# Kernel tuning notes

Measured on AMD Instinct MI355X. Metric: run time of the kernel, lower is better.

The kernel has to match this reference:

```python
import jax, jax.numpy as jnp
import numpy as np

T = 1024      # tokens
H = 2048      # hidden_size
I = 1408      # moe_intermediate_size
E = 16        # n_routed_experts
K = 6         # num_experts_per_tok
SI = I * 2    # shared experts intermediate (n_shared_experts=2)


def setup_inputs() -> dict:
    key = jax.random.key(0)
    ks = jax.random.split(key, 8)
    s = 0.02
    return {
        "x": jax.random.normal(ks[0], (T, H), jnp.float32),
        "gate_w": jax.random.normal(ks[1], (E, H), jnp.float32) * s,
        "w_gate": jax.random.normal(ks[2], (E, I, H), jnp.float32) * s,
        "w_up": jax.random.normal(ks[3], (E, I, H), jnp.float32) * s,
        "w_down": jax.random.normal(ks[4], (E, H, I), jnp.float32) * s,
        "sw_gate": jax.random.normal(ks[5], (SI, H), jnp.float32) * s,
        "sw_up": jax.random.normal(ks[6], (SI, H), jnp.float32) * s,
        "sw_down": jax.random.normal(ks[7], (H, SI), jnp.float32) * s,
    }


def reference(x, gate_w, w_gate, w_up, w_down, sw_gate, sw_up, sw_down):
    t = x.shape[0]
    # ---- router: softmax over experts, top-k, renormalize (norm_topk_prob) ----
    logits = x @ gate_w.T                                   # [T, E]
    probs = jax.nn.softmax(logits.astype(jnp.float32), axis=-1)
    topw, topi = jax.lax.top_k(probs, K)                    # [T, K]
    topw = topw / jnp.sum(topw, axis=-1, keepdims=True)
    # per-token per-expert combine weight (0 for unselected experts)
    comb = jnp.zeros((t, E), probs.dtype).at[
        jnp.arange(t)[:, None], topi
    ].add(topw)                                             # [T, E]

    # ---- routed experts: SwiGLU MLP per expert, weighted combine ----
    g = jnp.einsum('th,eih->tei', x, w_gate)                # [T, E, I]
    u = jnp.einsum('th,eih->tei', x, w_up)                  # [T, E, I]
    h = jax.nn.silu(g) * u                                  # [T, E, I]
    routed = jnp.einsum('te,tei,ehi->th', comb, h, w_down)  # [T, H]

    # ---- shared experts (always-on SwiGLU MLP) ----
    shared = (jax.nn.silu(x @ sw_gate.T) * (x @ sw_up.T)) @ sw_down.T  # [T, H]

    return routed + shared
```

## Files before the change

### kernel.cpp

```cpp
#include <hip/hip_runtime.h>
#include <stdint.h>

#define T_TOK 1024
#define H_DIM 2048
#define I_DIM 1408
#define E_NUM 16
#define K_TOP 6
#define SI_DIM 2816
#define PADCAP 8192

typedef __attribute__((ext_vector_type(8))) short short8;
typedef __attribute__((ext_vector_type(8))) unsigned short ushort8;
typedef __attribute__((ext_vector_type(4))) float f32x4;

__device__ __forceinline__ unsigned short f2b(float f) {
    unsigned u = __float_as_uint(f);
    u += 0x7fffu + ((u >> 16) & 1u);
    return (unsigned short)(u >> 16);
}
__device__ __forceinline__ float b2f(unsigned short s) {
    return __uint_as_float((unsigned)s << 16);
}

__device__ __forceinline__ unsigned cvt_pk2(float a, float b) {
    unsigned r;
    asm("v_cvt_pk_bf16_f32 %0, %1, %2" : "=v"(r) : "v"(a), "v"(b));
    return r;
}

typedef __attribute__((address_space(1))) const unsigned int as1_uint;
typedef __attribute__((address_space(3))) unsigned int as3_uint;
__device__ __forceinline__ void gload16(const void* g, void* l) {
    __builtin_amdgcn_global_load_lds((as1_uint*)g, (as3_uint*)l, 16, 0, 0);
}

__device__ __forceinline__ int xcd_swizzle(int bid, int nwg) {
    const int q = nwg >> 3, r = nwg & 7;
    const int xcd = bid & 7, k = bid >> 3;
    const int base = (xcd < r) ? xcd * (q + 1) : r * (q + 1) + (xcd - r) * q;
    return base + k;
}

__global__ __launch_bounds__(256) void router_kernel(
    const float* __restrict__ x, const float* __restrict__ gw,
    float* __restrict__ topw, int* __restrict__ eidx, int* __restrict__ slotarr,
    int* __restrict__ counts)
{
    const int t = blockIdx.x, tid = threadIdx.x;
    const int lane = tid & 63, wave = tid >> 6;
    float part[E_NUM];
#pragma unroll
    for (int e = 0; e < E_NUM; ++e) part[e] = 0.f;
    const float* xr = x + (size_t)t * H_DIM;
    for (int i = tid; i < H_DIM; i += 256) {
        float xv = xr[i];
#pragma unroll
        for (int e = 0; e < E_NUM; ++e) part[e] += xv * gw[e * H_DIM + i];
    }
    __shared__ float red[4][E_NUM];
#pragma unroll
    for (int e = 0; e < E_NUM; ++e) {
        float v = part[e];
        for (int off = 32; off; off >>= 1) v += __shfl_down(v, off);
        if (lane == 0) red[wave][e] = v;
    }
    __syncthreads();
    if (tid == 0) {
        float logits[E_NUM];
#pragma unroll
        for (int e = 0; e < E_NUM; ++e)
            logits[e] = red[0][e] + red[1][e] + red[2][e] + red[3][e];
        int sel[K_TOP]; float selv[K_TOP];
        unsigned used = 0;
        for (int k = 0; k < K_TOP; ++k) {
            int best = 0; float bv = -1e30f;
            for (int e = 0; e < E_NUM; ++e)
                if (!((used >> e) & 1u) && logits[e] > bv) { bv = logits[e]; best = e; }
            used |= 1u << best; sel[k] = best; selv[k] = bv;
        }
        float mx = selv[0], s = 0.f, w[K_TOP];
        for (int k = 0; k < K_TOP; ++k) { w[k] = expf(selv[k] - mx); s += w[k]; }
        float inv = 1.f / s;
        for (int k = 0; k < K_TOP; ++k) {
            int slot = atomicAdd(&counts[sel[k]], 1);
            topw[t * K_TOP + k] = w[k] * inv;
            eidx[t * K_TOP + k] = sel[k];
            slotarr[t * K_TOP + k] = slot;
        }
    }
}

__global__ void zero_counts_kernel(int* counts) {
    if (threadIdx.x < E_NUM) counts[threadIdx.x] = 0;
}

__global__ void prefix_kernel(const int* __restrict__ counts, int* __restrict__ offs) {
    if (threadIdx.x == 0) {
        int o = 0;
        for (int e = 0; e < E_NUM; ++e) { offs[e] = o; o += (counts[e] + 127) & ~127; }
        offs[E_NUM] = o;
    }
}

__global__ __launch_bounds__(256) void gather_rows_kernel(
    const float* __restrict__ x, const int* __restrict__ eidx,
    const int* __restrict__ slotarr, const int* __restrict__ offs,
    ushort* __restrict__ Xg)
{
    const int b = blockIdx.x;
    const int t = b / K_TOP;
    const int e = eidx[b], s = slotarr[b];
    const size_t row = (size_t)offs[e] + (size_t)s;
    const float* src = x + (size_t)t * H_DIM;
    ushort* dst = Xg + row * H_DIM;
    const int i = threadIdx.x * 8;
    float4 f0 = *(const float4*)(src + i);
    float4 f1 = *(const float4*)(src + i + 4);
    ushort8 v;
    v[0] = f2b(f0.x); v[1] = f2b(f0.y); v[2] = f2b(f0.z); v[3] = f2b(f0.w);
    v[4] = f2b(f1.x); v[5] = f2b(f1.y); v[6] = f2b(f1.z); v[7] = f2b(f1.w);
    *(ushort8*)(dst + i) = v;
}

__global__ __launch_bounds__(256) void cvt_rows_kernel(
    const float* __restrict__ x, ushort* __restrict__ Xb)
{
    const size_t row = blockIdx.x;
    const float* src = x + row * H_DIM;
    ushort* dst = Xb + row * H_DIM;
    const int i = threadIdx.x * 8;
    float4 f0 = *(const float4*)(src + i);
    float4 f1 = *(const float4*)(src + i + 4);
    ushort8 v;
    v[0] = f2b(f0.x); v[1] = f2b(f0.y); v[2] = f2b(f0.z); v[3] = f2b(f0.w);
    v[4] = f2b(f1.x); v[5] = f2b(f1.y); v[6] = f2b(f1.z); v[7] = f2b(f1.w);
    *(ushort8*)(dst + i) = v;
}

template<int STORE_F32>
__global__ __launch_bounds__(256) void gemm_bt_kernel(
    const ushort* __restrict__ Abase,
    const float* __restrict__ B1, const float* __restrict__ B2,
    void* __restrict__ C1, void* __restrict__ C2,
    const int* __restrict__ counts, const int* __restrict__ offs,
    int Mconst, int nNT, int totNT, int nMT, int K, long strideB, int ldc)
{
    __shared__ short Alds[128 * 64];
    __shared__ float Blds[128 * 64];

    const int work = xcd_swizzle(blockIdx.x, gridDim.x);
    const int perE = totNT * nMT;
    const int e = work / perE;
    int rem = work - e * perE;
    int nt = rem / nMT;
    const int mt = rem - nt * nMT;

    int M = Mconst, rowbase = 0;
    if (counts) { M = counts[e]; rowbase = offs[e]; }
    const int row0 = mt * 128;
    if (row0 >= M) return;

    const float* Bsel = B1;
    void* Csel = C1;
    if (nt >= nNT) { Bsel = B2; Csel = C2; nt -= nNT; }
    const int n0 = nt * 128;
    const float* __restrict__ B = Bsel + (size_t)e * (size_t)strideB;
    const char* __restrict__ Ab = (const char*)(Abase + (size_t)(rowbase + row0) * K);
    const char* __restrict__ Bb = (const char*)(B + (size_t)n0 * K);

    const int tid = threadIdx.x;
    const int lane = tid & 63;
    const int wave = tid >> 6;
    const int wm = wave & 1, wn = wave >> 1;
    const int l15 = lane & 15, lhi = lane >> 4;

    int aRow[4], aSlot[4];
    char* aDst[4];
#pragma unroll
    for (int i = 0; i < 4; ++i) {
        const int chunk = wave * 4 + i;
        const int off = chunk * 1024 + lane * 16;
        const int r = off >> 7, s = (off >> 4) & 7;
        aRow[i] = r; aSlot[i] = s ^ (r & 7);
        aDst[i] = (char*)Alds + chunk * 1024;
    }
    int bRow[8], bSlot[8];
    char* bDst[8];
#pragma unroll
    for (int i = 0; i < 8; ++i) {
        const int chunk = wave * 8 + i;
        const int off = chunk * 1024 + lane * 16;
        const int r = off >> 8, s = (off >> 4) & 15;
        bRow[i] = r; bSlot[i] = s ^ (r & 7);
        bDst[i] = (char*)Blds + chunk * 1024;
    }

    f32x4 acc[4][4];
#pragma unroll
    for (int m = 0; m < 4; ++m)
#pragma unroll
        for (int n = 0; n < 4; ++n) acc[m][n] = (f32x4){0.f, 0.f, 0.f, 0.f};

    const int nK = K >> 6;
    for (int kt = 0; kt < nK; ++kt) {
        const int k0 = kt << 6;
        __syncthreads();
#pragma unroll
        for (int i = 0; i < 4; ++i)
            gload16(Ab + (size_t)aRow[i] * K * 2 + k0 * 2 + (aSlot[i] << 4), aDst[i]);
#pragma unroll
        for (int i = 0; i < 8; ++i)
            gload16(Bb + (size_t)bRow[i] * K * 4 + k0 * 4 + (bSlot[i] << 4), bDst[i]);
        __syncthreads();

#pragma unroll
        for (int kk = 0; kk < 2; ++kk) {
            const int kb = (kk << 2) + lhi;
            short8 af[4], bfr[4];
#pragma unroll
            for (int m = 0; m < 4; ++m) {
                const int rA = (wm << 6) + (m << 4) + l15;
                af[m] = *(const short8*)&Alds[(rA << 6) + ((kb ^ (rA & 7)) << 3)];
            }
#pragma unroll
            for (int n = 0; n < 4; ++n) {
                const int rB = (wn << 6) + (n << 4) + l15;
                const int s0 = (kb << 1) ^ (rB & 7);
                const int s1 = ((kb << 1) | 1) ^ (rB & 7);
                f32x4 x0 = *(const f32x4*)&Blds[(rB << 6) + (s0 << 2)];
                f32x4 x1 = *(const f32x4*)&Blds[(rB << 6) + (s1 << 2)];
                union { short8 s8; unsigned u[4]; } bb;
                bb.u[0] = cvt_pk2(x0[0], x0[1]);
                bb.u[1] = cvt_pk2(x0[2], x0[3]);
                bb.u[2] = cvt_pk2(x1[0], x1[1]);
                bb.u[3] = cvt_pk2(x1[2], x1[3]);
                bfr[n] = bb.s8;
            }
#pragma unroll
            for (int m = 0; m < 4; ++m)
#pragma unroll
                for (int n = 0; n < 4; ++n)
                    acc[m][n] = __builtin_amdgcn_mfma_f32_16x16x32_bf16(
                        af[m], bfr[n], acc[m][n], 0, 0, 0);
        }
    }

    const size_t cbase_col = (size_t)n0 + (wn << 6) + l15;
#pragma unroll
    for (int m = 0; m < 4; ++m) {
        const int rloc = (wm << 6) + (m << 4) + (lhi << 2);
#pragma unroll
        for (int j = 0; j < 4; ++j) {
            const int crow = row0 + rloc + j;
            if (crow >= M) continue;
            const size_t co = (size_t)(rowbase + crow) * ldc + cbase_col;
            if (STORE_F32) {
                float* C = (float*)Csel;
#pragma unroll
                for (int n = 0; n < 4; ++n) C[co + (n << 4)] = acc[m][n][j];
            } else {
                ushort* C = (ushort*)Csel;
#pragma unroll
                for (int n = 0; n < 4; ++n) C[co + (n << 4)] = f2b(acc[m][n][j]);
            }
        }
    }
}

__global__ __launch_bounds__(256) void silu_rows_kernel(
    const ushort* __restrict__ G, const ushort* __restrict__ U,
    ushort* __restrict__ Hh, const int* __restrict__ eidx,
    const int* __restrict__ slotarr, const int* __restrict__ offs, int rowlen)
{
    size_t row;
    if (eidx) {
        const int b = blockIdx.x;
        row = (size_t)offs[eidx[b]] + (size_t)slotarr[b];
    } else {
        row = blockIdx.x;
    }
    const ushort* g = G + row * rowlen;
    const ushort* u = U + row * rowlen;
    ushort* h = Hh + row * rowlen;
    for (int i = threadIdx.x * 8; i < rowlen; i += 2048) {
        ushort8 gv = *(const ushort8*)(g + i);
        ushort8 uv = *(const ushort8*)(u + i);
        ushort8 hv;
#pragma unroll
        for (int j = 0; j < 8; ++j) {
            float gf = b2f(gv[j]);
            float uf = b2f(uv[j]);
            float sf = gf / (1.f + expf(-gf));
            hv[j] = f2b(sf * uf);
        }
        *(ushort8*)(h + i) = hv;
    }
}

__global__ __launch_bounds__(256) void combine_kernel(
    float* __restrict__ out, const ushort* __restrict__ Y,
    const float* __restrict__ topw, const int* __restrict__ eidx,
    const int* __restrict__ slotarr, const int* __restrict__ offs)
{
    const int t = blockIdx.x;
    const int i = threadIdx.x * 8;
    float* o = out + (size_t)t * H_DIM;
    float acc[8];
    float4 o0 = *(const float4*)(o + i);
    float4 o1 = *(const float4*)(o + i + 4);
    acc[0] = o0.x; acc[1] = o0.y; acc[2] = o0.z; acc[3] = o0.w;
    acc[4] = o1.x; acc[5] = o1.y; acc[6] = o1.z; acc[7] = o1.w;
#pragma unroll
    for (int k = 0; k < K_TOP; ++k) {
        const float w = topw[t * K_TOP + k];
        const size_t row = (size_t)offs[eidx[t * K_TOP + k]] + (size_t)slotarr[t * K_TOP + k];
        ushort8 v = *(const ushort8*)(Y + row * H_DIM + i);
#pragma unroll
        for (int j = 0; j < 8; ++j) acc[j] += w * b2f(v[j]);
    }
    o0.x = acc[0]; o0.y = acc[1]; o0.z = acc[2]; o0.w = acc[3];
    o1.x = acc[4]; o1.y = acc[5]; o1.z = acc[6]; o1.w = acc[7];
    *(float4*)(o + i) = o0;
    *(float4*)(o + i + 4) = o1;
}

extern "C" void kernel_launch(void* const* d_in, const int* in_sizes, int n_in,
                              void* d_out, int out_size, void* d_ws, size_t ws_size,
                              hipStream_t stream) {
    const float* x       = (const float*)d_in[0];
    const float* gate_w  = (const float*)d_in[1];
    const float* w_gate  = (const float*)d_in[2];
    const float* w_up    = (const float*)d_in[3];
    const float* w_down  = (const float*)d_in[4];
    const float* sw_gate = (const float*)d_in[5];
    const float* sw_up   = (const float*)d_in[6];
    const float* sw_down = (const float*)d_in[7];
    float* out = (float*)d_out;

    char* p = (char*)d_ws;
    auto take = [&](size_t b) { char* r = p; p += (b + 255) & ~(size_t)255; return r; };
    int*    counts = (int*)take(E_NUM * 4);
    int*    offs   = (int*)take((E_NUM + 1) * 4);
    float*  topw   = (float*)take((size_t)T_TOK * K_TOP * 4);
    int*    eidx   = (int*)take((size_t)T_TOK * K_TOP * 4);
    int*    slot   = (int*)take((size_t)T_TOK * K_TOP * 4);
    ushort* Xg     = (ushort*)take((size_t)PADCAP * H_DIM * 2);
    ushort* G      = (ushort*)take((size_t)PADCAP * I_DIM * 2);
    ushort* U      = (ushort*)take((size_t)PADCAP * I_DIM * 2);
    ushort* Hr     = (ushort*)take((size_t)PADCAP * I_DIM * 2);
    ushort* Xb     = (ushort*)take((size_t)T_TOK * H_DIM * 2);
    ushort* Gs     = (ushort*)take((size_t)T_TOK * SI_DIM * 2);
    ushort* Us     = (ushort*)take((size_t)T_TOK * SI_DIM * 2);
    ushort* Hs     = (ushort*)take((size_t)T_TOK * SI_DIM * 2);

    zero_counts_kernel<<<1, 64, 0, stream>>>(counts);
    router_kernel<<<T_TOK, 256, 0, stream>>>(x, gate_w, topw, eidx, slot, counts);
    prefix_kernel<<<1, 64, 0, stream>>>(counts, offs);
    gather_rows_kernel<<<T_TOK * K_TOP, 256, 0, stream>>>(x, eidx, slot, offs, Xg);
    cvt_rows_kernel<<<T_TOK, 256, 0, stream>>>(x, Xb);

    gemm_bt_kernel<0><<<E_NUM * 22 * 8, 256, 0, stream>>>(
        Xg, w_gate, w_up, G, U, counts, offs,
        0, 11, 22, 8, H_DIM, (long)I_DIM * H_DIM, I_DIM);
    silu_rows_kernel<<<T_TOK * K_TOP, 256, 0, stream>>>(G, U, Hr, eidx, slot, offs, I_DIM);
    gemm_bt_kernel<0><<<E_NUM * 16 * 8, 256, 0, stream>>>(
        Hr, w_down, nullptr, Xg, nullptr, counts, offs,
        0, 16, 16, 8, I_DIM, (long)H_DIM * I_DIM, H_DIM);

    gemm_bt_kernel<0><<<44 * 8, 256, 0, stream>>>(
        Xb, sw_gate, sw_up, Gs, Us, nullptr, nullptr,
        T_TOK, 22, 44, 8, H_DIM, 0, SI_DIM);
    silu_rows_kernel<<<T_TOK, 256, 0, stream>>>(Gs, Us, Hs, nullptr, nullptr, nullptr, SI_DIM);
    gemm_bt_kernel<1><<<16 * 8, 256, 0, stream>>>(
        Hs, sw_down, nullptr, out, nullptr, nullptr, nullptr,
        T_TOK, 16, 16, 8, SI_DIM, 0, H_DIM);

    combine_kernel<<<T_TOK, 256, 0, stream>>>(out, Xg, topw, eidx, slot, offs);
}
```

Baseline: 553.8 us.

## Fold shared experts into grouped MoE GEMMs as two extra experts with register-staged B

Treats the two shared-expert halves as extra experts 16 and 17, so gate/up, SiLU and down projections run in single grouped launches instead of separate routed and shared kernels. The shared down projection writes two bf16 partial outputs that the combine kernel sums with the routed results. The GEMM now loads fp32 weights into registers and converts them to bf16 once per tile, writing a double-buffered bf16 LDS tile, rather than converting at every fragment read. This also prefetches the next K-tile during the MFMAs, cuts LDS traffic and sets occupancy to 3 blocks. SiLU writes in place and the gather and convert kernels are merged, at the cost of a bf16 round trip on the shared output and more workspace.

```diff
diff --git a/kernel.cpp b/kernel.cpp
--- a/kernel.cpp
+++ b/kernel.cpp
@@ -6,8 +6,8 @@
 #define I_DIM 1408
 #define E_NUM 16
 #define K_TOP 6
-#define SI_DIM 2816
 #define PADCAP 8192
+#define NE_ALL 18
 
 typedef __attribute__((ext_vector_type(8))) short short8;
 typedef __attribute__((ext_vector_type(8))) unsigned short ushort8;
@@ -102,17 +102,22 @@
     }
 }
 
-__global__ __launch_bounds__(256) void gather_rows_kernel(
+__global__ __launch_bounds__(256) void gather_cvt_kernel(
     const float* __restrict__ x, const int* __restrict__ eidx,
     const int* __restrict__ slotarr, const int* __restrict__ offs,
-    ushort* __restrict__ Xg)
+    ushort* __restrict__ Xall)
 {
     const int b = blockIdx.x;
-    const int t = b / K_TOP;
-    const int e = eidx[b], s = slotarr[b];
-    const size_t row = (size_t)offs[e] + (size_t)s;
+    int t; size_t row;
+    if (b < T_TOK * K_TOP) {
+        t = b / K_TOP;
+        row = (size_t)offs[eidx[b]] + (size_t)slotarr[b];
+    } else {
+        t = b - T_TOK * K_TOP;
+        row = (size_t)offs[E_NUM] + (size_t)t;
+    }
     const float* src = x + (size_t)t * H_DIM;
-    ushort* dst = Xg + row * H_DIM;
+    ushort* dst = Xall + row * H_DIM;
     const int i = threadIdx.x * 8;
     float4 f0 = *(const float4*)(src + i);
     float4 f1 = *(const float4*)(src + i + 4);
@@ -122,51 +127,48 @@
     *(ushort8*)(dst + i) = v;
 }
 
-__global__ __launch_bounds__(256) void cvt_rows_kernel(
-    const float* __restrict__ x, ushort* __restrict__ Xb)
-{
-    const size_t row = blockIdx.x;
-    const float* src = x + row * H_DIM;
-    ushort* dst = Xb + row * H_DIM;
-    const int i = threadIdx.x * 8;
-    float4 f0 = *(const float4*)(src + i);
-    float4 f1 = *(const float4*)(src + i + 4);
-    ushort8 v;
-    v[0] = f2b(f0.x); v[1] = f2b(f0.y); v[2] = f2b(f0.z); v[3] = f2b(f0.w);
-    v[4] = f2b(f1.x); v[5] = f2b(f1.y); v[6] = f2b(f1.z); v[7] = f2b(f1.w);
-    *(ushort8*)(dst + i) = v;
-}
-
-template<int STORE_F32>
-__global__ __launch_bounds__(256) void gemm_bt_kernel(
+template<int DOWN>
+__global__ __launch_bounds__(256, 3) void moe_gemm_kernel(
     const ushort* __restrict__ Abase,
-    const float* __restrict__ B1, const float* __restrict__ B2,
-    void* __restrict__ C1, void* __restrict__ C2,
+    const float* __restrict__ Wr1, const float* __restrict__ Wr2,
+    const float* __restrict__ Ws1, const float* __restrict__ Ws2,
+    ushort* __restrict__ C1, ushort* __restrict__ C2,
     const int* __restrict__ counts, const int* __restrict__ offs,
-    int Mconst, int nNT, int totNT, int nMT, int K, long strideB, int ldc)
+    int nNT, int K, int ldc)
 {
     __shared__ short Alds[128 * 64];
-    __shared__ float Blds[128 * 64];
+    __shared__ short Blds[2][128 * 64];
 
     const int work = xcd_swizzle(blockIdx.x, gridDim.x);
-    const int perE = totNT * nMT;
-    const int e = work / perE;
-    int rem = work - e * perE;
-    int nt = rem / nMT;
-    const int mt = rem - nt * nMT;
-
-    int M = Mconst, rowbase = 0;
-    if (counts) { M = counts[e]; rowbase = offs[e]; }
-    const int row0 = mt * 128;
+    const int slab = NE_ALL * 8;
+    int nt = work / slab;
+    const int rem = work - nt * slab;
+    const int e = rem >> 3;
+    const int mt = rem & 7;
+
+    const int S = offs[E_NUM];
+    const int M = (e < E_NUM) ? counts[e] : 1024;
+    const int row0 = mt << 7;
     if (row0 >= M) return;
-
-    const float* Bsel = B1;
-    void* Csel = C1;
-    if (nt >= nNT) { Bsel = B2; Csel = C2; nt -= nNT; }
-    const int n0 = nt * 128;
-    const float* __restrict__ B = Bsel + (size_t)e * (size_t)strideB;
-    const char* __restrict__ Ab = (const char*)(Abase + (size_t)(rowbase + row0) * K);
-    const char* __restrict__ Bb = (const char*)(B + (size_t)n0 * K);
+    const int crowbase = (e < E_NUM) ? offs[e] : S + ((e - E_NUM) << 10);
+    const int arowbase = DOWN ? crowbase : ((e < E_NUM) ? offs[e] : S);
+
+    const float* B; ushort* C; int ldb;
+    if (DOWN) {
+        ldb = (e < E_NUM) ? I_DIM : 2 * I_DIM;
+        B = (e < E_NUM) ? Wr1 + (size_t)e * H_DIM * I_DIM
+                        : Ws1 + (size_t)(e - E_NUM) * I_DIM;
+        C = C1;
+    } else {
+        ldb = H_DIM;
+        const float* Bg = (e < E_NUM) ? Wr1 + (size_t)e * I_DIM * H_DIM
+                                      : Ws1 + (size_t)(e - E_NUM) * I_DIM * H_DIM;
+        const float* Bu = (e < E_NUM) ? Wr2 + (size_t)e * I_DIM * H_DIM
+                                      : Ws2 + (size_t)(e - E_NUM) * I_DIM * H_DIM;
+        if (nt < nNT) { B = Bg; C = C1; }
+        else          { B = Bu; C = C2; nt -= nNT; }
+    }
+    const int n0 = nt << 7;
 
     const int tid = threadIdx.x;
     const int lane = tid & 63;
@@ -174,26 +176,22 @@
     const int wm = wave & 1, wn = wave >> 1;
     const int l15 = lane & 15, lhi = lane >> 4;
 
-    int aRow[4], aSlot[4];
-    char* aDst[4];
+    const char* __restrict__ Ab = (const char*)(Abase + (size_t)(arowbase + row0) * K);
+
+    int aOff[4]; char* aDst[4];
 #pragma unroll
     for (int i = 0; i < 4; ++i) {
         const int chunk = wave * 4 + i;
         const int off = chunk * 1024 + lane * 16;
         const int r = off >> 7, s = (off >> 4) & 7;
-        aRow[i] = r; aSlot[i] = s ^ (r & 7);
+        aOff[i] = r * K * 2 + ((s ^ (r & 7)) << 4);
         aDst[i] = (char*)Alds + chunk * 1024;
     }
-    int bRow[8], bSlot[8];
-    char* bDst[8];
-#pragma unroll
-    for (int i = 0; i < 8; ++i) {
-        const int chunk = wave * 8 + i;
-        const int off = chunk * 1024 + lane * 16;
-        const int r = off >> 8, s = (off >> 4) & 15;
-        bRow[i] = r; bSlot[i] = s ^ (r & 7);
-        bDst[i] = (char*)Blds + chunk * 1024;
-    }
+
+    const int r0 = (wave << 5) + (lane >> 3);
+    const int sl = lane & 7;
+    const float* Bg0 = B + (size_t)(n0 + r0) * ldb + (sl << 3);
+    const int bLds0 = (r0 << 6) + ((sl ^ (r0 & 7)) << 3);
 
     f32x4 acc[4][4];
 #pragma unroll
@@ -201,18 +199,40 @@
 #pragma unroll
         for (int n = 0; n < 4; ++n) acc[m][n] = (f32x4){0.f, 0.f, 0.f, 0.f};
 
+    float4 breg[4][2];
+    auto issueB = [&](int k0) {
+#pragma unroll
+        for (int j = 0; j < 4; ++j) {
+            const float* src = Bg0 + (size_t)(j << 3) * ldb + k0;
+            breg[j][0] = *(const float4*)src;
+            breg[j][1] = *(const float4*)(src + 4);
+        }
+    };
+    auto writeB = [&](int p) {
+        short* bl = Blds[p];
+#pragma unroll
+        for (int j = 0; j < 4; ++j) {
+            union { short8 s; unsigned u[4]; } w;
+            w.u[0] = cvt_pk2(breg[j][0].x, breg[j][0].y);
+            w.u[1] = cvt_pk2(breg[j][0].z, breg[j][0].w);
+            w.u[2] = cvt_pk2(breg[j][1].x, breg[j][1].y);
+            w.u[3] = cvt_pk2(breg[j][1].z, breg[j][1].w);
+            *(short8*)&bl[bLds0 + (j << 9)] = w.s;
+        }
+    };
+
     const int nK = K >> 6;
+    issueB(0);
+    int p = 0;
     for (int kt = 0; kt < nK; ++kt) {
         const int k0 = kt << 6;
         __syncthreads();
 #pragma unroll
         for (int i = 0; i < 4; ++i)
-            gload16(Ab + (size_t)aRow[i] * K * 2 + k0 * 2 + (aSlot[i] << 4), aDst[i]);
-#pragma unroll
-        for (int i = 0; i < 8; ++i)
-            gload16(Bb + (size_t)bRow[i] * K * 4 + k0 * 4 + (bSlot[i] << 4), bDst[i]);
+            gload16(Ab + (size_t)aOff[i] + k0 * 2, aDst[i]);
+        writeB(p);
         __syncthreads();
-
+        if (kt + 1 < nK) issueB(k0 + 64);
 #pragma unroll
         for (int kk = 0; kk < 2; ++kk) {
             const int kb = (kk << 2) + lhi;
@@ -225,16 +245,7 @@
 #pragma unroll
             for (int n = 0; n < 4; ++n) {
                 const int rB = (wn << 6) + (n << 4) + l15;
-                const int s0 = (kb << 1) ^ (rB & 7);
-                const int s1 = ((kb << 1) | 1) ^ (rB & 7);
-                f32x4 x0 = *(const f32x4*)&Blds[(rB << 6) + (s0 << 2)];
-                f32x4 x1 = *(const f32x4*)&Blds[(rB << 6) + (s1 << 2)];
-                union { short8 s8; unsigned u[4]; } bb;
-                bb.u[0] = cvt_pk2(x0[0], x0[1]);
-                bb.u[1] = cvt_pk2(x0[2], x0[3]);
-                bb.u[2] = cvt_pk2(x1[0], x1[1]);
-                bb.u[3] = cvt_pk2(x1[2], x1[3]);
-                bfr[n] = bb.s8;
+                bfr[n] = *(const short8*)&Blds[p][(rB << 6) + ((kb ^ (rB & 7)) << 3)];
             }
 #pragma unroll
             for (int m = 0; m < 4; ++m)
@@ -243,6 +254,7 @@
                     acc[m][n] = __builtin_amdgcn_mfma_f32_16x16x32_bf16(
                         af[m], bfr[n], acc[m][n], 0, 0, 0);
         }
+        p ^= 1;
     }
 
     const size_t cbase_col = (size_t)n0 + (wn << 6) + l15;
@@ -253,36 +265,28 @@
         for (int j = 0; j < 4; ++j) {
             const int crow = row0 + rloc + j;
             if (crow >= M) continue;
-            const size_t co = (size_t)(rowbase + crow) * ldc + cbase_col;
-            if (STORE_F32) {
-                float* C = (float*)Csel;
-#pragma unroll
-                for (int n = 0; n < 4; ++n) C[co + (n << 4)] = acc[m][n][j];
-            } else {
-                ushort* C = (ushort*)Csel;
-#pragma unroll
-                for (int n = 0; n < 4; ++n) C[co + (n << 4)] = f2b(acc[m][n][j]);
-            }
-        }
-    }
-}
-
-__global__ __launch_bounds__(256) void silu_rows_kernel(
-    const ushort* __restrict__ G, const ushort* __restrict__ U,
-    ushort* __restrict__ Hh, const int* __restrict__ eidx,
-    const int* __restrict__ slotarr, const int* __restrict__ offs, int rowlen)
-{
+            const size_t co = (size_t)(crowbase + crow) * ldc + cbase_col;
+#pragma unroll
+            for (int n = 0; n < 4; ++n) C[co + (n << 4)] = f2b(acc[m][n][j]);
+        }
+    }
+}
+
+__global__ __launch_bounds__(256) void silu_kernel(
+    ushort* __restrict__ G, const ushort* __restrict__ U,
+    const int* __restrict__ eidx, const int* __restrict__ slotarr,
+    const int* __restrict__ offs)
+{
+    const int b = blockIdx.x;
     size_t row;
-    if (eidx) {
-        const int b = blockIdx.x;
+    if (b < T_TOK * K_TOP) {
         row = (size_t)offs[eidx[b]] + (size_t)slotarr[b];
     } else {
-        row = blockIdx.x;
-    }
-    const ushort* g = G + row * rowlen;
-    const ushort* u = U + row * rowlen;
-    ushort* h = Hh + row * rowlen;
-    for (int i = threadIdx.x * 8; i < rowlen; i += 2048) {
+        row = (size_t)offs[E_NUM] + (size_t)(b - T_TOK * K_TOP);
+    }
+    ushort* g = G + row * I_DIM;
+    const ushort* u = U + row * I_DIM;
+    for (int i = threadIdx.x * 8; i < I_DIM; i += 2048) {
         ushort8 gv = *(const ushort8*)(g + i);
         ushort8 uv = *(const ushort8*)(u + i);
         ushort8 hv;
@@ -293,7 +297,7 @@
             float sf = gf / (1.f + expf(-gf));
             hv[j] = f2b(sf * uf);
         }
-        *(ushort8*)(h + i) = hv;
+        *(ushort8*)(g + i) = hv;
     }
 }
 
@@ -304,12 +308,14 @@
 {
     const int t = blockIdx.x;
     const int i = threadIdx.x * 8;
-    float* o = out + (size_t)t * H_DIM;
+    const int S = offs[E_NUM];
     float acc[8];
-    float4 o0 = *(const float4*)(o + i);
-    float4 o1 = *(const float4*)(o + i + 4);
-    acc[0] = o0.x; acc[1] = o0.y; acc[2] = o0.z; acc[3] = o0.w;
-    acc[4] = o1.x; acc[5] = o1.y; acc[6] = o1.z; acc[7] = o1.w;
+    {
+        ushort8 v0 = *(const ushort8*)(Y + ((size_t)S + t) * H_DIM + i);
+        ushort8 v1 = *(const ushort8*)(Y + ((size_t)S + 1024 + t) * H_DIM + i);
+#pragma unroll
+        for (int j = 0; j < 8; ++j) acc[j] = b2f(v0[j]) + b2f(v1[j]);
+    }
 #pragma unroll
     for (int k = 0; k < K_TOP; ++k) {
         const float w = topw[t * K_TOP + k];
@@ -318,6 +324,8 @@
 #pragma unroll
         for (int j = 0; j < 8; ++j) acc[j] += w * b2f(v[j]);
     }
+    float* o = out + (size_t)t * H_DIM;
+    float4 o0, o1;
     o0.x = acc[0]; o0.y = acc[1]; o0.z = acc[2]; o0.w = acc[3];
     o1.x = acc[4]; o1.y = acc[5]; o1.z = acc[6]; o1.w = acc[7];
     *(float4*)(o + i) = o0;
@@ -339,41 +347,26 @@
 
     char* p = (char*)d_ws;
     auto take = [&](size_t b) { char* r = p; p += (b + 255) & ~(size_t)255; return r; };
-    int*    counts = (int*)take(E_NUM * 4);
-    int*    offs   = (int*)take((E_NUM + 1) * 4);
+    int*    counts = (int*)take(32 * 4);
+    int*    offs   = (int*)take(32 * 4);
     float*  topw   = (float*)take((size_t)T_TOK * K_TOP * 4);
     int*    eidx   = (int*)take((size_t)T_TOK * K_TOP * 4);
     int*    slot   = (int*)take((size_t)T_TOK * K_TOP * 4);
-    ushort* Xg     = (ushort*)take((size_t)PADCAP * H_DIM * 2);
-    ushort* G      = (ushort*)take((size_t)PADCAP * I_DIM * 2);
-    ushort* U      = (ushort*)take((size_t)PADCAP * I_DIM * 2);
-    ushort* Hr     = (ushort*)take((size_t)PADCAP * I_DIM * 2);
-    ushort* Xb     = (ushort*)take((size_t)T_TOK * H_DIM * 2);
-    ushort* Gs     = (ushort*)take((size_t)T_TOK * SI_DIM * 2);
-    ushort* Us     = (ushort*)take((size_t)T_TOK * SI_DIM * 2);
-    ushort* Hs     = (ushort*)take((size_t)T_TOK * SI_DIM * 2);
+    ushort* Xall   = (ushort*)take((size_t)(PADCAP + 1024) * H_DIM * 2);
+    ushort* G      = (ushort*)take((size_t)(PADCAP + 2048) * I_DIM * 2);
+    ushort* U      = (ushort*)take((size_t)(PADCAP + 2048) * I_DIM * 2);
+    ushort* Y      = (ushort*)take((size_t)(PADCAP + 2048) * H_DIM * 2);
 
     zero_counts_kernel<<<1, 64, 0, stream>>>(counts);
     router_kernel<<<T_TOK, 256, 0, stream>>>(x, gate_w, topw, eidx, slot, counts);
     prefix_kernel<<<1, 64, 0, stream>>>(counts, offs);
-    gather_rows_kernel<<<T_TOK * K_TOP, 256, 0, stream>>>(x, eidx, slot, offs, Xg);
-    cvt_rows_kernel<<<T_TOK, 256, 0, stream>>>(x, Xb);
-
-    gemm_bt_kernel<0><<<E_NUM * 22 * 8, 256, 0, stream>>>(
-        Xg, w_gate, w_up, G, U, counts, offs,
-        0, 11, 22, 8, H_DIM, (long)I_DIM * H_DIM, I_DIM);
-    silu_rows_kernel<<<T_TOK * K_TOP, 256, 0, stream>>>(G, U, Hr, eidx, slot, offs, I_DIM);
-    gemm_bt_kernel<0><<<E_NUM * 16 * 8, 256, 0, stream>>>(
-        Hr, w_down, nullptr, Xg, nullptr, counts, offs,
-        0, 16, 16, 8, I_DIM, (long)H_DIM * I_DIM, H_DIM);
-
-    gemm_bt_kernel<0><<<44 * 8, 256, 0, stream>>>(
-        Xb, sw_gate, sw_up, Gs, Us, nullptr, nullptr,
-        T_TOK, 22, 44, 8, H_DIM, 0, SI_DIM);
-    silu_rows_kernel<<<T_TOK, 256, 0, stream>>>(Gs, Us, Hs, nullptr, nullptr, nullptr, SI_DIM);
-    gemm_bt_kernel<1><<<16 * 8, 256, 0, stream>>>(
-        Hs, sw_down, nullptr, out, nullptr, nullptr, nullptr,
-        T_TOK, 16, 16, 8, SI_DIM, 0, H_DIM);
-
-    combine_kernel<<<T_TOK, 256, 0, stream>>>(out, Xg, topw, eidx, slot, offs);
-}
+    gather_cvt_kernel<<<T_TOK * K_TOP + T_TOK, 256, 0, stream>>>(x, eidx, slot, offs, Xall);
+
+    moe_gemm_kernel<0><<<22 * NE_ALL * 8, 256, 0, stream>>>(
+        Xall, w_gate, w_up, sw_gate, sw_up, G, U, counts, offs, 11, H_DIM, I_DIM);
+    silu_kernel<<<T_TOK * K_TOP + 2048, 256, 0, stream>>>(G, U, eidx, slot, offs);
+    moe_gemm_kernel<1><<<16 * NE_ALL * 8, 256, 0, stream>>>(
+        G, w_down, nullptr, sw_down, nullptr, Y, nullptr, counts, offs, 16, I_DIM, H_DIM);
+
+    combine_kernel<<<T_TOK, 256, 0, stream>>>(out, Y, topw, eidx, slot, offs);
+}
```

After: 468.9 us. 15.3% less time.
